# Kernel tuning notes

Hardware: AMD Instinct MI355X
Metric: run time of the kernel (lower is better)

The kernel has to match this reference:

```python
import jax, jax.numpy as jnp
import numpy as np

B, D, N, H = 2, 512, 2048, 8
DK = D // H
EPS = 1e-5


def conv1x1(x, w, b):
    # kernel-size-1 Conv1d == channel-mixing GEMM: (o,i) x (b,i,n) -> (b,o,n)
    return jnp.einsum('oi,bin->bon', w, x) + b[None, :, None]


def setup_inputs() -> dict:
    key = jax.random.key(0)
    ks = jax.random.split(key, 20)
    s = 0.02
    return {
        'init_query': jax.random.normal(ks[0], (B, D, N), jnp.float32),
        'key_t': jax.random.normal(ks[1], (B, D, N), jnp.float32),
        'value': jax.random.normal(ks[2], (B, D, N), jnp.float32),
        'mask': jax.random.randint(ks[3], (B, 1, N, N), 0, 2, jnp.int32),
        'Wq': jax.random.normal(ks[4], (D, D), jnp.float32) * s,
        'bq': jax.random.normal(ks[5], (D,), jnp.float32) * s,
        'Wk': jax.random.normal(ks[6], (D, D), jnp.float32) * s,
        'bk': jax.random.normal(ks[7], (D,), jnp.float32) * s,
        'Wv': jax.random.normal(ks[8], (D, D), jnp.float32) * s,
        'bv': jax.random.normal(ks[9], (D,), jnp.float32) * s,
        'Wm': jax.random.normal(ks[10], (D, D), jnp.float32) * s,
        'bm': jax.random.normal(ks[11], (D,), jnp.float32) * s,
        'W1': jax.random.normal(ks[12], (2 * D, 2 * D), jnp.float32) * s,
        'b1': jax.random.normal(ks[13], (2 * D,), jnp.float32) * s,
        'gamma': jnp.ones((2 * D,), jnp.float32),
        'beta': jnp.zeros((2 * D,), jnp.float32),
        'rmean': jax.random.normal(ks[14], (2 * D,), jnp.float32) * s,
        'rvar': jnp.abs(jax.random.normal(ks[15], (2 * D,), jnp.float32)) * 0.1 + 0.5,
        'W2': jax.random.normal(ks[16], (D, 2 * D), jnp.float32) * s,
        'b2': jnp.zeros((D,), jnp.float32),  # nn.init.constant_(bias, 0.0)
    }


def reference(init_query, key_t, value, mask, Wq, bq, Wk, bk, Wv, bv, Wm, bm,
              W1, b1, gamma, beta, rmean, rvar, W2, b2):
    # projections, split channels into (d_k, n_heads) exactly like torch .view
    q = conv1x1(init_query, Wq, bq).reshape(B, DK, H, N)
    k = conv1x1(key_t, Wk, bk).reshape(B, DK, H, N)
    v = conv1x1(value, Wv, bv).reshape(B, DK, H, N)
    scores = jnp.einsum('bdhn,bdhm->bhnm', q, k) / jnp.sqrt(jnp.float32(DK))
    scores = jnp.where(mask == 0, jnp.float32(-1e9), scores)
    attn = jax.nn.softmax(scores, axis=-1)
    x = jnp.einsum('bhnm,bdhm->bdhn', attn, v).reshape(B, D, N)
    x = conv1x1(x, Wm, bm)
    x = jnp.concatenate([x, init_query], axis=1)  # (B, 2D, N)
    h = conv1x1(x, W1, b1)
    # BatchNorm1d (inference mode with running stats) + ReLU
    h = (h - rmean[None, :, None]) * (gamma / jnp.sqrt(rvar + EPS))[None, :, None] + beta[None, :, None]
    h = jax.nn.relu(h)
    return conv1x1(h, W2, b2)
```

## Files before the change

### kernel.cpp

```cpp
#include <hip/hip_runtime.h>

typedef unsigned short u16;
typedef unsigned int u32;
typedef unsigned long long u64;
typedef long long i64;
typedef __bf16 bf16x8 __attribute__((ext_vector_type(8)));
typedef float f32x4 __attribute__((ext_vector_type(4)));

#define DEV __device__ __forceinline__

constexpr int BB = 2, DD = 512, NN = 2048, HH = 8, DKc = 64, D2 = 1024;

constexpr float QSC = 0.125f * 1.44269504088896340736f;

constexpr i64 OFF_CAT = 0;
constexpr i64 OFF_XKT = 8388608;
constexpr i64 OFF_XVT = 12582912;
constexpr i64 OFF_OP0 = 8388608;
constexpr i64 OFF_QH  = 16777216;
constexpr i64 OFF_KH  = 20971520;
constexpr i64 OFF_VT  = 25165824;
constexpr i64 OFF_OT  = 29360128;
constexpr i64 OFF_HT  = 33554432;
constexpr i64 OFF_OP1 = 33554432;
constexpr i64 OFF_WQP = 41943040;
constexpr i64 OFF_WKP = 42467328;
constexpr i64 OFF_WVP = 42991616;
constexpr i64 OFF_WMP = 43515904;
constexpr i64 OFF_W1B = 44040192;
constexpr i64 OFF_W2B = 46137344;
constexpr i64 OFF_BQP = 47185920;
constexpr i64 OFF_BKP = 47187968;
constexpr i64 OFF_BVP = 47190016;
constexpr i64 OFF_BNA = 47192064;
constexpr i64 OFF_BNC = 47196160;
constexpr i64 OFF_MSK = 47200256;
constexpr i64 OFF_LP  = 48248832;

DEV u16 f2bf(float f) {
  u32 u = __float_as_uint(f);
  u = u + 0x7FFFu + ((u >> 16) & 1u);
  return (u16)(u >> 16);
}

DEV float bf2f(u16 u) { return __uint_as_float(((u32)u) << 16); }

DEV bf16x8 ldfrag(const u16* p) {
  bf16x8 v;
  __builtin_memcpy(&v, __builtin_assume_aligned(p, 16), 16);
  return v;
}

DEV bf16x8 ldfrag8(const u16* p) {
  bf16x8 v;
  __builtin_memcpy(&v, __builtin_assume_aligned(p, 8), 16);
  return v;
}

DEV void gload16(const void* g, void* lds) {
  __builtin_amdgcn_global_load_lds((__attribute__((address_space(1))) void*)g,
                                   (__attribute__((address_space(3))) void*)lds, 16, 0, 0);
}

DEV f32x4 mfma16(bf16x8 a, bf16x8 b, f32x4 c) {
  return __builtin_amdgcn_mfma_f32_16x16x32_bf16(a, b, c, 0, 0, 0);
}

__global__ __launch_bounds__(256) void prep_kernel(
    const float* __restrict__ Wq, const float* __restrict__ Wk, const float* __restrict__ Wv,
    const float* __restrict__ Wm, const float* __restrict__ W1, const float* __restrict__ W2,
    const float* __restrict__ bq, const float* __restrict__ bk, const float* __restrict__ bv,
    const float* __restrict__ b1, const float* __restrict__ gamma_, const float* __restrict__ beta_,
    const float* __restrict__ rmean, const float* __restrict__ rvar, const int* __restrict__ mask,
    u16* __restrict__ wqp, u16* __restrict__ wkp, u16* __restrict__ wvp, u16* __restrict__ wmp,
    u16* __restrict__ w1b, u16* __restrict__ w2b,
    float* __restrict__ bqp, float* __restrict__ bkp, float* __restrict__ bvp,
    float* __restrict__ bna, float* __restrict__ bnc, u32* __restrict__ mw) {
  const int blk = blockIdx.x, t = threadIdx.x;
  if (blk < 768) {
    const int which = blk >> 8, lb = blk & 255;
    const float* W = which == 0 ? Wq : (which == 1 ? Wk : Wv);
    u16* dst = which == 0 ? wqp : (which == 1 ? wkp : wvp);
    for (int e = lb * 256 + t; e < 262144; e += 65536) {
      int op = e >> 9, i = e & 511;
      int dk = op & 63, h = op >> 6;
      dst[e] = f2bf(W[(dk * 8 + h) * 512 + i]);
    }
  } else if (blk < 1024) {
    const int lb = blk - 768;
    for (int e = lb * 256 + t; e < 262144; e += 65536) {
      int o = e >> 9, c = e & 511;
      int dk = c & 63, h = c >> 6;
      wmp[e] = f2bf(Wm[o * 512 + dk * 8 + h]);
    }
  } else if (blk < 1536) {
    const int lb = blk - 1024;
    for (int e = lb * 256 + t; e < 1048576; e += 131072) w1b[e] = f2bf(W1[e]);
  } else if (blk < 1792) {
    const int lb = blk - 1536;
    for (int e = lb * 256 + t; e < 524288; e += 65536) w2b[e] = f2bf(W2[e]);
  } else if (blk == 1792) {
    for (int e = t; e < 512; e += 256) {
      int src = (e & 63) * 8 + (e >> 6);
      bqp[e] = bq[src]; bkp[e] = bk[src]; bvp[e] = bv[src];
    }
    for (int e = t; e < 1024; e += 256) {
      float a = gamma_[e] * rsqrtf(rvar[e] + 1e-5f);
      bna[e] = a;
      bnc[e] = (b1[e] - rmean[e]) * a + beta_[e];
    }
  } else {
    const int tid = (blk - 1793) * 256 + t;
    const i64 base = (i64)tid * 32;
    const int4* mp = (const int4*)(mask + base);
    u32 word = 0;
#pragma unroll
    for (int j = 0; j < 8; ++j) {
      int4 x = mp[j];
      u32 nib = (x.x != 0 ? 1u : 0u) | (x.y != 0 ? 2u : 0u) | (x.z != 0 ? 4u : 0u) |
                (x.w != 0 ? 8u : 0u);
      word |= nib << (j * 4);
    }
    mw[tid] = word;
  }
}

__global__ __launch_bounds__(256) void transpose_cvt(const float* __restrict__ iq,
                                                     const float* __restrict__ kt,
                                                     const float* __restrict__ vv,
                                                     u16* __restrict__ cat, u16* __restrict__ xkt,
                                                     u16* __restrict__ xvt) {
  __shared__ float tile[32][33];
  const int z = blockIdx.z, tensor = z >> 1, b = z & 1;
  const float* src = tensor == 0 ? iq : (tensor == 1 ? kt : vv);
  src += (i64)b * DD * NN;
  u16* dst; i64 ldd; int coff;
  if (tensor == 0)      { dst = cat + (i64)b * NN * D2; ldd = D2; coff = DD; }
  else if (tensor == 1) { dst = xkt + (i64)b * NN * DD; ldd = DD; coff = 0; }
  else                  { dst = xvt + (i64)b * NN * DD; ldd = DD; coff = 0; }
  const int x0 = blockIdx.x * 32, y0 = blockIdx.y * 32;
  const int col = threadIdx.x & 31, rg = threadIdx.x >> 5;
#pragma unroll
  for (int i = 0; i < 4; ++i) {
    int row = rg + i * 8;
    tile[row][col] = src[(i64)(y0 + row) * NN + x0 + col];
  }
  __syncthreads();
#pragma unroll
  for (int i = 0; i < 4; ++i) {
    int rr = rg + i * 8;
    dst[(i64)(x0 + rr) * ldd + coff + y0 + col] = f2bf(tile[col][rr]);
  }
}

struct GArgs {
  const u16* A; i64 lda, sAb;
  const u16* B; i64 ldb, sBb;
  void* C; i64 ldc, sCb;
  const float* p1; const float* p2;
  int K; float sc;
};

template <int MODE>
__global__ __launch_bounds__(256) void gemm_bt(GArgs g) {
  __shared__ __align__(16) u16 As[128 * 64];
  __shared__ __align__(16) u16 Bs[64 * 64];
  const int t = threadIdx.x;
  const int w = t >> 6, l = t & 63, quad = l >> 4, l15 = l & 15;
  const int wm = (w >> 1) * 64, wn = (w & 1) * 32;
  const int bz = blockIdx.z;
  const u16* A = g.A + (i64)bz * g.sAb + (i64)blockIdx.x * 128 * g.lda;
  const u16* Bp = g.B + (i64)bz * g.sBb + (i64)blockIdx.y * 64 * g.ldb;
  f32x4 acc[4][2] = {};
  for (int kk = 0; kk < g.K; kk += 64) {
    __syncthreads();
#pragma unroll
    for (int j = 0; j < 4; ++j) {
      int ch = j * 256 + w * 64 + l, r = ch >> 3, c = ch & 7;
      gload16(A + (i64)r * g.lda + kk + ((c ^ (r & 7)) << 3), &As[(j * 256 + w * 64) * 8]);
    }
#pragma unroll
    for (int j = 0; j < 2; ++j) {
      int ch = j * 256 + w * 64 + l, r = ch >> 3, c = ch & 7;
      gload16(Bp + (i64)r * g.ldb + kk + ((c ^ (r & 7)) << 3), &Bs[(j * 256 + w * 64) * 8]);
    }
    __syncthreads();
#pragma unroll
    for (int kc = 0; kc < 2; ++kc) {
      const int sw = ((kc * 4 + quad) ^ (l15 & 7)) << 3;
      bf16x8 af[4], bfr[2];
#pragma unroll
      for (int i = 0; i < 4; ++i) af[i] = ldfrag(&As[(wm + i * 16 + l15) * 64 + sw]);
#pragma unroll
      for (int j = 0; j < 2; ++j) bfr[j] = ldfrag(&Bs[(wn + j * 16 + l15) * 64 + sw]);
#pragma unroll
      for (int i = 0; i < 4; ++i)
#pragma unroll
        for (int j = 0; j < 2; ++j) acc[i][j] = mfma16(af[i], bfr[j], acc[i][j]);
    }
  }
  const int rowBase = blockIdx.x * 128 + wm + quad * 4;
  const int colBase = blockIdx.y * 64 + wn + l15;
#pragma unroll
  for (int j = 0; j < 2; ++j) {
    const int col = colBase + j * 16;
    float cA = 0.f, cB = 0.f;
    if (MODE == 0 || MODE == 1) cA = g.p1[col];
    if (MODE == 3) { cA = g.p1[col]; cB = g.p2[col]; }
#pragma unroll
    for (int i = 0; i < 4; ++i) {
#pragma unroll
      for (int r = 0; r < 4; ++r) {
        const int row = rowBase + i * 16 + r;
        float v = acc[i][j][r];
        if (MODE == 0) {
          ((u16*)g.C + (i64)bz * g.sCb)[(i64)row * g.ldc + col] = f2bf(v + cA);
        } else if (MODE == 1) {
          ((u16*)g.C + (i64)bz * g.sCb)[(i64)(col >> 6) * (NN * 64) + (i64)row * 64 + (col & 63)] =
              f2bf((v + cA) * g.sc);
        } else if (MODE == 2) {
          ((u16*)g.C + (i64)bz * g.sCb)[(i64)row * g.ldc + col] = f2bf(v + g.p1[row]);
        } else if (MODE == 3) {
          float x = v * cA + cB;
          ((u16*)g.C + (i64)bz * g.sCb)[(i64)row * g.ldc + col] = f2bf(x > 0.f ? x : 0.f);
        } else {
          ((float*)g.C + (i64)bz * g.sCb)[(i64)row * g.ldc + col] = v + g.p1[row];
        }
      }
    }
  }
}

__global__ __launch_bounds__(256) void flash_attn(const u16* __restrict__ Qh,
                                                  const u16* __restrict__ Kh,
                                                  const u16* __restrict__ Vt,
                                                  const u64* __restrict__ MW,
                                                  float* __restrict__ Op0, float* __restrict__ Op1,
                                                  float* __restrict__ Lp) {
  __shared__ __align__(16) u16 Qs[64 * 64];
  __shared__ __align__(16) u16 Ks[64 * 64];
  __shared__ __align__(16) u16 Vs[64 * 64];
  __shared__ __align__(16) u16 Ps[4][16 * 68];
  const int t = threadIdx.x, w = t >> 6, l = t & 63, quad = l >> 4, l15 = l & 15;
  const int nt = blockIdx.x, h = blockIdx.y, zz = blockIdx.z, b = zz >> 1, sp = zz & 1;
  const u16* Qb = Qh + ((i64)(b * HH + h) * NN + nt * 64) * 64;
  const u16* Kb = Kh + (i64)(b * HH + h) * NN * 64;
  const u16* Vb = Vt + (i64)(b * HH + h) * 64 * NN;
#pragma unroll
  for (int j = 0; j < 2; ++j) {
    int ch = j * 256 + w * 64 + l, r = ch >> 3, c = ch & 7;
    gload16(Qb + r * 64 + ((c ^ (r & 7)) << 3), &Qs[(j * 256 + w * 64) * 8]);
  }
  __syncthreads();
  bf16x8 qf[2];
#pragma unroll
  for (int kc = 0; kc < 2; ++kc)
    qf[kc] = ldfrag(&Qs[(w * 16 + l15) * 64 + (((kc * 4 + quad) ^ (l15 & 7)) << 3)]);

  f32x4 oacc[4] = {};
  float lacc[4] = {0.f, 0.f, 0.f, 0.f};
  const int mt0 = sp * 16, mt1 = mt0 + 16;
  for (int mt = mt0; mt < mt1; ++mt) {
    __syncthreads();
#pragma unroll
    for (int j = 0; j < 2; ++j) {
      int ch = j * 256 + w * 64 + l, r = ch >> 3, c = ch & 7;
      gload16(Kb + (i64)mt * 4096 + r * 64 + ((c ^ (r & 7)) << 3), &Ks[(j * 256 + w * 64) * 8]);
      gload16(Vb + (i64)r * NN + mt * 64 + ((c ^ (r & 7)) << 3), &Vs[(j * 256 + w * 64) * 8]);
    }
    __syncthreads();
    f32x4 s[4];
#pragma unroll
    for (int ct = 0; ct < 4; ++ct) {
      const int sw = l15 & 7;
      bf16x8 k0 = ldfrag(&Ks[(ct * 16 + l15) * 64 + ((quad ^ sw) << 3)]);
      bf16x8 k1 = ldfrag(&Ks[(ct * 16 + l15) * 64 + (((4 + quad) ^ sw) << 3)]);
      f32x4 z = {};
      z = mfma16(qf[0], k0, z);
      z = mfma16(qf[1], k1, z);
      s[ct] = z;
    }
    u64 mrow[4];
#pragma unroll
    for (int r = 0; r < 4; ++r) {
      int n = nt * 64 + w * 16 + quad * 4 + r;
      mrow[r] = MW[(i64)(b * NN + n) * 32 + mt];
    }
#pragma unroll
    for (int ct = 0; ct < 4; ++ct)
#pragma unroll
      for (int r = 0; r < 4; ++r) {
        float p = ((mrow[r] >> (ct * 16 + l15)) & 1ull) ? exp2f(s[ct][r]) : 0.f;
        lacc[r] += p;
        Ps[w][(quad * 4 + r) * 68 + ct * 16 + l15] = f2bf(p);
      }
    asm volatile("" ::: "memory");
    bf16x8 pf0 = ldfrag8(&Ps[w][l15 * 68 + quad * 8]);
    bf16x8 pf1 = ldfrag8(&Ps[w][l15 * 68 + 32 + quad * 8]);
#pragma unroll
    for (int dt = 0; dt < 4; ++dt) {
      const int sw = l15 & 7;
      bf16x8 v0 = ldfrag(&Vs[(dt * 16 + l15) * 64 + ((quad ^ sw) << 3)]);
      bf16x8 v1 = ldfrag(&Vs[(dt * 16 + l15) * 64 + (((4 + quad) ^ sw) << 3)]);
      oacc[dt] = mfma16(pf0, v0, oacc[dt]);
      oacc[dt] = mfma16(pf1, v1, oacc[dt]);
    }
  }
#pragma unroll
  for (int off = 1; off < 16; off <<= 1)
#pragma unroll
    for (int r = 0; r < 4; ++r) lacc[r] += __shfl_xor(lacc[r], off);
  float* Op = sp ? Op1 : Op0;
#pragma unroll
  for (int dt = 0; dt < 4; ++dt)
#pragma unroll
    for (int r = 0; r < 4; ++r) {
      int n = nt * 64 + w * 16 + quad * 4 + r;
      Op[((i64)(b * HH + h) * NN + n) * 64 + dt * 16 + l15] = oacc[dt][r];
    }
  if (l15 == 0) {
#pragma unroll
    for (int r = 0; r < 4; ++r) {
      int n = nt * 64 + w * 16 + quad * 4 + r;
      Lp[(i64)sp * BB * HH * NN + (i64)(b * HH + h) * NN + n] = lacc[r];
    }
  }
}

__global__ __launch_bounds__(256) void combine(const float* __restrict__ Op0,
                                               const float* __restrict__ Op1,
                                               const float* __restrict__ Lp,
                                               u16* __restrict__ Ot) {
  int idx = blockIdx.x * 256 + threadIdx.x;
  int b = idx >> 20, rem = idx & ((1 << 20) - 1);
  int n = rem >> 9, ch = rem & 511, h = ch >> 6, dk = ch & 63;
  i64 o = ((i64)(b * HH + h) * NN + n) * 64 + dk;
  float l0 = Lp[(i64)(b * HH + h) * NN + n];
  float l1 = Lp[(i64)BB * HH * NN + (i64)(b * HH + h) * NN + n];
  Ot[(i64)(b * NN + n) * DD + ch] = f2bf((Op0[o] + Op1[o]) / (l0 + l1));
}

extern "C" void kernel_launch(void* const* d_in, const int* in_sizes, int n_in,
                              void* d_out, int out_size, void* d_ws, size_t ws_size,
                              hipStream_t stream) {
  (void)in_sizes; (void)n_in; (void)out_size; (void)ws_size;
  const float* iq    = (const float*)d_in[0];
  const float* kt    = (const float*)d_in[1];
  const float* vv    = (const float*)d_in[2];
  const int*   mask  = (const int*)d_in[3];
  const float* Wq    = (const float*)d_in[4];
  const float* bq    = (const float*)d_in[5];
  const float* Wk    = (const float*)d_in[6];
  const float* bk    = (const float*)d_in[7];
  const float* Wv    = (const float*)d_in[8];
  const float* bv    = (const float*)d_in[9];
  const float* Wm    = (const float*)d_in[10];
  const float* bm    = (const float*)d_in[11];
  const float* W1    = (const float*)d_in[12];
  const float* b1    = (const float*)d_in[13];
  const float* gamma_= (const float*)d_in[14];
  const float* beta_ = (const float*)d_in[15];
  const float* rmean = (const float*)d_in[16];
  const float* rvar  = (const float*)d_in[17];
  const float* W2    = (const float*)d_in[18];
  const float* b2    = (const float*)d_in[19];

  char* ws = (char*)d_ws;
  u16* cat = (u16*)(ws + OFF_CAT);
  u16* xkt = (u16*)(ws + OFF_XKT);
  u16* xvt = (u16*)(ws + OFF_XVT);
  u16* qh  = (u16*)(ws + OFF_QH);
  u16* kh  = (u16*)(ws + OFF_KH);
  u16* vt  = (u16*)(ws + OFF_VT);
  u16* ot  = (u16*)(ws + OFF_OT);
  u16* ht  = (u16*)(ws + OFF_HT);
  u16* wqp = (u16*)(ws + OFF_WQP);
  u16* wkp = (u16*)(ws + OFF_WKP);
  u16* wvp = (u16*)(ws + OFF_WVP);
  u16* wmp = (u16*)(ws + OFF_WMP);
  u16* w1b = (u16*)(ws + OFF_W1B);
  u16* w2b = (u16*)(ws + OFF_W2B);
  float* bqp = (float*)(ws + OFF_BQP);
  float* bkp = (float*)(ws + OFF_BKP);
  float* bvp = (float*)(ws + OFF_BVP);
  float* bna = (float*)(ws + OFF_BNA);
  float* bnc = (float*)(ws + OFF_BNC);
  u32* mw = (u32*)(ws + OFF_MSK);
  float* op0 = (float*)(ws + OFF_OP0);
  float* op1 = (float*)(ws + OFF_OP1);
  float* lp  = (float*)(ws + OFF_LP);

  prep_kernel<<<2817, 256, 0, stream>>>(Wq, Wk, Wv, Wm, W1, W2, bq, bk, bv, b1, gamma_, beta_,
                                        rmean, rvar, mask, wqp, wkp, wvp, wmp, w1b, w2b,
                                        bqp, bkp, bvp, bna, bnc, mw);
  transpose_cvt<<<dim3(64, 16, 6), 256, 0, stream>>>(iq, kt, vv, cat, xkt, xvt);

  GArgs qa{cat + DD, D2, (i64)NN * D2, wqp, DD, 0, qh, 0, (i64)HH * NN * DKc, bqp, nullptr, DD, QSC};
  gemm_bt<1><<<dim3(16, 8, 2), 256, 0, stream>>>(qa);
  GArgs ka{xkt, DD, (i64)NN * DD, wkp, DD, 0, kh, 0, (i64)HH * NN * DKc, bkp, nullptr, DD, 1.f};
  gemm_bt<1><<<dim3(16, 8, 2), 256, 0, stream>>>(ka);
  GArgs va{wvp, DD, 0, xvt, DD, (i64)NN * DD, vt, NN, (i64)HH * DKc * NN, bvp, nullptr, DD, 1.f};
  gemm_bt<2><<<dim3(4, 32, 2), 256, 0, stream>>>(va);

  flash_attn<<<dim3(32, 8, 4), 256, 0, stream>>>(qh, kh, vt, (const u64*)mw, op0, op1, lp);
  combine<<<8192, 256, 0, stream>>>(op0, op1, lp, ot);

  GArgs ma{ot, DD, (i64)NN * DD, wmp, DD, 0, cat, D2, (i64)NN * D2, bm, nullptr, DD, 1.f};
  gemm_bt<0><<<dim3(16, 8, 2), 256, 0, stream>>>(ma);
  GArgs wa{cat, D2, (i64)NN * D2, w1b, D2, 0, ht, D2, (i64)NN * D2, bna, bnc, D2, 1.f};
  gemm_bt<3><<<dim3(16, 16, 2), 256, 0, stream>>>(wa);
  GArgs w2a{w2b, D2, 0, ht, D2, (i64)NN * D2, d_out, NN, (i64)DD * NN, b2, nullptr, D2, 1.f};
  gemm_bt<4><<<dim3(4, 32, 2), 256, 0, stream>>>(w2a);
}
```

Measured before the change: 262.0 us.

## Fuse QKV GEMMs, drop attention split-K combine, compute row sums via MFMA

The three Q/K/V projection GEMMs become one launch indexed by blockIdx.z. Flash attention no longer splits the key range in two, so it drops the fp32 partial outputs and the separate combine kernel and writes normalized bf16 output directly. Inside attention, masking is applied with packed bitwise ANDs on bf16 pairs. Row sums of P are now taken with an MFMA against a ones vector instead of a shuffle reduction. The V output uses a permuted column layout to allow vector stores of P, and the Wm and W2 GEMMs use smaller tiles for more blocks. In exchange, attention has half as many blocks, each with a loop twice as long.

```diff
diff --git a/kernel.cpp b/kernel.cpp
--- a/kernel.cpp
+++ b/kernel.cpp
@@ -5,6 +5,8 @@
 typedef unsigned long long u64;
 typedef long long i64;
 typedef __bf16 bf16x8 __attribute__((ext_vector_type(8)));
+typedef u16 u16x8 __attribute__((ext_vector_type(8)));
+typedef u32 u32x2 __attribute__((ext_vector_type(2)));
 typedef float f32x4 __attribute__((ext_vector_type(4)));
 
 #define DEV __device__ __forceinline__
@@ -16,13 +18,11 @@
 constexpr i64 OFF_CAT = 0;
 constexpr i64 OFF_XKT = 8388608;
 constexpr i64 OFF_XVT = 12582912;
-constexpr i64 OFF_OP0 = 8388608;
 constexpr i64 OFF_QH  = 16777216;
 constexpr i64 OFF_KH  = 20971520;
 constexpr i64 OFF_VT  = 25165824;
 constexpr i64 OFF_OT  = 29360128;
 constexpr i64 OFF_HT  = 33554432;
-constexpr i64 OFF_OP1 = 33554432;
 constexpr i64 OFF_WQP = 41943040;
 constexpr i64 OFF_WKP = 42467328;
 constexpr i64 OFF_WVP = 42991616;
@@ -35,7 +35,6 @@
 constexpr i64 OFF_BNA = 47192064;
 constexpr i64 OFF_BNC = 47196160;
 constexpr i64 OFF_MSK = 47200256;
-constexpr i64 OFF_LP  = 48248832;
 
 DEV u16 f2bf(float f) {
   u32 u = __float_as_uint(f);
@@ -43,7 +42,17 @@
   return (u16)(u >> 16);
 }
 
-DEV float bf2f(u16 u) { return __uint_as_float(((u32)u) << 16); }
+DEV u32 packbf(float lo, float hi) {
+  return __builtin_amdgcn_perm(__float_as_uint(hi), __float_as_uint(lo), 0x07060302u);
+}
+
+DEV float fexp2(float x) {
+#if __has_builtin(__builtin_amdgcn_exp2f)
+  return __builtin_amdgcn_exp2f(x);
+#else
+  return exp2f(x);
+#endif
+}
 
 DEV bf16x8 ldfrag(const u16* p) {
   bf16x8 v;
@@ -54,6 +63,13 @@
 DEV bf16x8 ldfrag8(const u16* p) {
   bf16x8 v;
   __builtin_memcpy(&v, __builtin_assume_aligned(p, 8), 16);
+  return v;
+}
+
+DEV bf16x8 ones8() {
+  u16x8 u = {0x3F80, 0x3F80, 0x3F80, 0x3F80, 0x3F80, 0x3F80, 0x3F80, 0x3F80};
+  bf16x8 v;
+  __builtin_memcpy(&v, &u, 16);
   return v;
 }
 
@@ -153,73 +169,148 @@
   }
 }
 
+template <int AM, int AN>
+DEV void gemm_core(const u16* __restrict__ A, i64 lda, const u16* __restrict__ Bp, i64 ldb,
+                   int K, u16* As, u16* Bs, f32x4 (&acc)[AM][AN]) {
+  constexpr int BM = AM * 32, BN = AN * 32;
+  const int t = threadIdx.x, w = t >> 6, l = t & 63, quad = l >> 4, l15 = l & 15;
+  const int wm = (w >> 1) * AM * 16, wn = (w & 1) * AN * 16;
+  for (int kk = 0; kk < K; kk += 64) {
+    __syncthreads();
+#pragma unroll
+    for (int j = 0; j < BM / 32; ++j) {
+      int ch = j * 256 + w * 64 + l, r = ch >> 3, c = ch & 7;
+      gload16(A + (i64)r * lda + kk + ((c ^ (r & 7)) << 3), As + (j * 256 + w * 64) * 8);
+    }
+#pragma unroll
+    for (int j = 0; j < BN / 32; ++j) {
+      int ch = j * 256 + w * 64 + l, r = ch >> 3, c = ch & 7;
+      gload16(Bp + (i64)r * ldb + kk + ((c ^ (r & 7)) << 3), Bs + (j * 256 + w * 64) * 8);
+    }
+    __syncthreads();
+#pragma unroll
+    for (int kc = 0; kc < 2; ++kc) {
+      const int sw = ((kc * 4 + quad) ^ (l15 & 7)) << 3;
+      bf16x8 af[AM], bfr[AN];
+#pragma unroll
+      for (int i = 0; i < AM; ++i) af[i] = ldfrag(&As[(wm + i * 16 + l15) * 64 + sw]);
+#pragma unroll
+      for (int j = 0; j < AN; ++j) bfr[j] = ldfrag(&Bs[(wn + j * 16 + l15) * 64 + sw]);
+#pragma unroll
+      for (int i = 0; i < AM; ++i)
+#pragma unroll
+        for (int j = 0; j < AN; ++j) acc[i][j] = mfma16(af[i], bfr[j], acc[i][j]);
+    }
+  }
+}
+
+__global__ __launch_bounds__(256) void qkv_gemm(const u16* __restrict__ cat,
+                                                const u16* __restrict__ xkt,
+                                                const u16* __restrict__ xvt,
+                                                const u16* __restrict__ wqp,
+                                                const u16* __restrict__ wkp,
+                                                const u16* __restrict__ wvp,
+                                                const float* __restrict__ bqp,
+                                                const float* __restrict__ bkp,
+                                                const float* __restrict__ bvp,
+                                                u16* __restrict__ qh, u16* __restrict__ kh,
+                                                u16* __restrict__ vt) {
+  __shared__ __align__(16) u16 As[128 * 64];
+  __shared__ __align__(16) u16 Bs[64 * 64];
+  const int z = blockIdx.z, op = z >> 1, b = z & 1;
+  const int t = threadIdx.x, w = t >> 6, l = t & 63, quad = l >> 4, l15 = l & 15;
+  const int wm = (w >> 1) * 64, wn = (w & 1) * 32;
+  int mx, ny;
+  const u16 *A, *Bp;
+  i64 lda, ldb;
+  if (op < 2) {
+    mx = blockIdx.x; ny = blockIdx.y;
+    A = (op == 0 ? cat + DD : xkt);
+    lda = (op == 0 ? D2 : DD);
+    A += (i64)b * NN * lda + (i64)mx * 128 * lda;
+    Bp = (op == 0 ? wqp : wkp) + (i64)ny * 64 * DD;
+    ldb = DD;
+  } else {
+    int f = blockIdx.x * 8 + blockIdx.y;
+    mx = f >> 5; ny = f & 31;
+    A = wvp + (i64)mx * 128 * DD; lda = DD;
+    Bp = xvt + (i64)b * NN * DD + (i64)ny * 64 * DD; ldb = DD;
+  }
+  f32x4 acc[4][2] = {};
+  gemm_core<4, 2>(A, lda, Bp, ldb, DD, As, Bs, acc);
+
+  const int rowBase = mx * 128 + wm + quad * 4;
+  const int colBase = ny * 64 + wn + l15;
+  if (op < 2) {
+    const float* bias = (op == 0 ? bqp : bkp);
+    const float sc = (op == 0 ? QSC : 1.f);
+    u16* dst = (op == 0 ? qh : kh) + (i64)b * HH * NN * DKc;
+#pragma unroll
+    for (int j = 0; j < 2; ++j) {
+      const int col = colBase + j * 16;
+      const float cA = bias[col];
+#pragma unroll
+      for (int i = 0; i < 4; ++i)
+#pragma unroll
+        for (int r = 0; r < 4; ++r) {
+          const int row = rowBase + i * 16 + r;
+          dst[(i64)(col >> 6) * (NN * 64) + (i64)row * 64 + (col & 63)] =
+              f2bf((acc[i][j][r] + cA) * sc);
+        }
+    }
+  } else {
+    u16* dst = vt + (i64)b * HH * DKc * NN;
+#pragma unroll
+    for (int j = 0; j < 2; ++j) {
+      const int col = colBase + j * 16;
+      const int colp = (col & ~63) | (((col & 15) << 2) | ((col >> 4) & 3));
+#pragma unroll
+      for (int i = 0; i < 4; ++i)
+#pragma unroll
+        for (int r = 0; r < 4; ++r) {
+          const int row = rowBase + i * 16 + r;
+          dst[(i64)row * NN + colp] = f2bf(acc[i][j][r] + bvp[row]);
+        }
+    }
+  }
+}
+
 struct GArgs {
   const u16* A; i64 lda, sAb;
   const u16* B; i64 ldb, sBb;
   void* C; i64 ldc, sCb;
   const float* p1; const float* p2;
-  int K; float sc;
+  int K;
 };
 
-template <int MODE>
+template <int MODE, int AM, int AN>
 __global__ __launch_bounds__(256) void gemm_bt(GArgs g) {
-  __shared__ __align__(16) u16 As[128 * 64];
-  __shared__ __align__(16) u16 Bs[64 * 64];
-  const int t = threadIdx.x;
-  const int w = t >> 6, l = t & 63, quad = l >> 4, l15 = l & 15;
-  const int wm = (w >> 1) * 64, wn = (w & 1) * 32;
+  __shared__ __align__(16) u16 As[AM * 32 * 64];
+  __shared__ __align__(16) u16 Bs[AN * 32 * 64];
+  const int t = threadIdx.x, w = t >> 6, l = t & 63, quad = l >> 4, l15 = l & 15;
+  const int wm = (w >> 1) * AM * 16, wn = (w & 1) * AN * 16;
   const int bz = blockIdx.z;
-  const u16* A = g.A + (i64)bz * g.sAb + (i64)blockIdx.x * 128 * g.lda;
-  const u16* Bp = g.B + (i64)bz * g.sBb + (i64)blockIdx.y * 64 * g.ldb;
-  f32x4 acc[4][2] = {};
-  for (int kk = 0; kk < g.K; kk += 64) {
-    __syncthreads();
-#pragma unroll
-    for (int j = 0; j < 4; ++j) {
-      int ch = j * 256 + w * 64 + l, r = ch >> 3, c = ch & 7;
-      gload16(A + (i64)r * g.lda + kk + ((c ^ (r & 7)) << 3), &As[(j * 256 + w * 64) * 8]);
-    }
-#pragma unroll
-    for (int j = 0; j < 2; ++j) {
-      int ch = j * 256 + w * 64 + l, r = ch >> 3, c = ch & 7;
-      gload16(Bp + (i64)r * g.ldb + kk + ((c ^ (r & 7)) << 3), &Bs[(j * 256 + w * 64) * 8]);
-    }
-    __syncthreads();
-#pragma unroll
-    for (int kc = 0; kc < 2; ++kc) {
-      const int sw = ((kc * 4 + quad) ^ (l15 & 7)) << 3;
-      bf16x8 af[4], bfr[2];
-#pragma unroll
-      for (int i = 0; i < 4; ++i) af[i] = ldfrag(&As[(wm + i * 16 + l15) * 64 + sw]);
-#pragma unroll
-      for (int j = 0; j < 2; ++j) bfr[j] = ldfrag(&Bs[(wn + j * 16 + l15) * 64 + sw]);
-#pragma unroll
-      for (int i = 0; i < 4; ++i)
-#pragma unroll
-        for (int j = 0; j < 2; ++j) acc[i][j] = mfma16(af[i], bfr[j], acc[i][j]);
-    }
-  }
-  const int rowBase = blockIdx.x * 128 + wm + quad * 4;
-  const int colBase = blockIdx.y * 64 + wn + l15;
-#pragma unroll
-  for (int j = 0; j < 2; ++j) {
+  const u16* A = g.A + (i64)bz * g.sAb + (i64)blockIdx.x * (AM * 32) * g.lda;
+  const u16* Bp = g.B + (i64)bz * g.sBb + (i64)blockIdx.y * (AN * 32) * g.ldb;
+  f32x4 acc[AM][AN] = {};
+  gemm_core<AM, AN>(A, g.lda, Bp, g.ldb, g.K, As, Bs, acc);
+
+  const int rowBase = blockIdx.x * (AM * 32) + wm + quad * 4;
+  const int colBase = blockIdx.y * (AN * 32) + wn + l15;
+#pragma unroll
+  for (int j = 0; j < AN; ++j) {
     const int col = colBase + j * 16;
     float cA = 0.f, cB = 0.f;
-    if (MODE == 0 || MODE == 1) cA = g.p1[col];
+    if (MODE == 0) cA = g.p1[col];
     if (MODE == 3) { cA = g.p1[col]; cB = g.p2[col]; }
 #pragma unroll
-    for (int i = 0; i < 4; ++i) {
+    for (int i = 0; i < AM; ++i) {
 #pragma unroll
       for (int r = 0; r < 4; ++r) {
         const int row = rowBase + i * 16 + r;
         float v = acc[i][j][r];
         if (MODE == 0) {
           ((u16*)g.C + (i64)bz * g.sCb)[(i64)row * g.ldc + col] = f2bf(v + cA);
-        } else if (MODE == 1) {
-          ((u16*)g.C + (i64)bz * g.sCb)[(i64)(col >> 6) * (NN * 64) + (i64)row * 64 + (col & 63)] =
-              f2bf((v + cA) * g.sc);
-        } else if (MODE == 2) {
-          ((u16*)g.C + (i64)bz * g.sCb)[(i64)row * g.ldc + col] = f2bf(v + g.p1[row]);
         } else if (MODE == 3) {
           float x = v * cA + cB;
           ((u16*)g.C + (i64)bz * g.sCb)[(i64)row * g.ldc + col] = f2bf(x > 0.f ? x : 0.f);
@@ -235,17 +326,17 @@
                                                   const u16* __restrict__ Kh,
                                                   const u16* __restrict__ Vt,
                                                   const u64* __restrict__ MW,
-                                                  float* __restrict__ Op0, float* __restrict__ Op1,
-                                                  float* __restrict__ Lp) {
+                                                  u16* __restrict__ Ot) {
   __shared__ __align__(16) u16 Qs[64 * 64];
   __shared__ __align__(16) u16 Ks[64 * 64];
   __shared__ __align__(16) u16 Vs[64 * 64];
   __shared__ __align__(16) u16 Ps[4][16 * 68];
   const int t = threadIdx.x, w = t >> 6, l = t & 63, quad = l >> 4, l15 = l & 15;
-  const int nt = blockIdx.x, h = blockIdx.y, zz = blockIdx.z, b = zz >> 1, sp = zz & 1;
+  const int nt = blockIdx.x, h = blockIdx.y, b = blockIdx.z;
   const u16* Qb = Qh + ((i64)(b * HH + h) * NN + nt * 64) * 64;
   const u16* Kb = Kh + (i64)(b * HH + h) * NN * 64;
   const u16* Vb = Vt + (i64)(b * HH + h) * 64 * NN;
+  const bf16x8 ONE = ones8();
 #pragma unroll
   for (int j = 0; j < 2; ++j) {
     int ch = j * 256 + w * 64 + l, r = ch >> 3, c = ch & 7;
@@ -258,9 +349,8 @@
     qf[kc] = ldfrag(&Qs[(w * 16 + l15) * 64 + (((kc * 4 + quad) ^ (l15 & 7)) << 3)]);
 
   f32x4 oacc[4] = {};
-  float lacc[4] = {0.f, 0.f, 0.f, 0.f};
-  const int mt0 = sp * 16, mt1 = mt0 + 16;
-  for (int mt = mt0; mt < mt1; ++mt) {
+  f32x4 lacc = {};
+  for (int mt = 0; mt < NN / 64; ++mt) {
     __syncthreads();
 #pragma unroll
     for (int j = 0; j < 2; ++j) {
@@ -280,23 +370,22 @@
       z = mfma16(qf[1], k1, z);
       s[ct] = z;
     }
-    u64 mrow[4];
 #pragma unroll
     for (int r = 0; r < 4; ++r) {
       int n = nt * 64 + w * 16 + quad * 4 + r;
-      mrow[r] = MW[(i64)(b * NN + n) * 32 + mt];
-    }
-#pragma unroll
-    for (int ct = 0; ct < 4; ++ct)
-#pragma unroll
-      for (int r = 0; r < 4; ++r) {
-        float p = ((mrow[r] >> (ct * 16 + l15)) & 1ull) ? exp2f(s[ct][r]) : 0.f;
-        lacc[r] += p;
-        Ps[w][(quad * 4 + r) * 68 + ct * 16 + l15] = f2bf(p);
-      }
+      u64 sh = MW[(i64)(b * NN + n) * 32 + mt] >> l15;
+      u32 m01 = ((u32)sh & 0x00010001u) * 0xFFFFu;
+      u32 m23 = ((u32)(sh >> 32) & 0x00010001u) * 0xFFFFu;
+      u32 w0 = packbf(fexp2(s[0][r]), fexp2(s[1][r])) & m01;
+      u32 w1 = packbf(fexp2(s[2][r]), fexp2(s[3][r])) & m23;
+      u32x2 pair = {w0, w1};
+      __builtin_memcpy(__builtin_assume_aligned(&Ps[w][(quad * 4 + r) * 68 + l15 * 4], 8), &pair, 8);
+    }
     asm volatile("" ::: "memory");
     bf16x8 pf0 = ldfrag8(&Ps[w][l15 * 68 + quad * 8]);
     bf16x8 pf1 = ldfrag8(&Ps[w][l15 * 68 + 32 + quad * 8]);
+    lacc = mfma16(pf0, ONE, lacc);
+    lacc = mfma16(pf1, ONE, lacc);
 #pragma unroll
     for (int dt = 0; dt < 4; ++dt) {
       const int sw = l15 & 7;
@@ -306,38 +395,16 @@
       oacc[dt] = mfma16(pf1, v1, oacc[dt]);
     }
   }
-#pragma unroll
-  for (int off = 1; off < 16; off <<= 1)
-#pragma unroll
-    for (int r = 0; r < 4; ++r) lacc[r] += __shfl_xor(lacc[r], off);
-  float* Op = sp ? Op1 : Op0;
+  float inv[4];
+#pragma unroll
+  for (int r = 0; r < 4; ++r) inv[r] = __builtin_amdgcn_rcpf(lacc[r]);
 #pragma unroll
   for (int dt = 0; dt < 4; ++dt)
 #pragma unroll
     for (int r = 0; r < 4; ++r) {
       int n = nt * 64 + w * 16 + quad * 4 + r;
-      Op[((i64)(b * HH + h) * NN + n) * 64 + dt * 16 + l15] = oacc[dt][r];
-    }
-  if (l15 == 0) {
-#pragma unroll
-    for (int r = 0; r < 4; ++r) {
-      int n = nt * 64 + w * 16 + quad * 4 + r;
-      Lp[(i64)sp * BB * HH * NN + (i64)(b * HH + h) * NN + n] = lacc[r];
-    }
-  }
-}
-
-__global__ __launch_bounds__(256) void combine(const float* __restrict__ Op0,
-                                               const float* __restrict__ Op1,
-                                               const float* __restrict__ Lp,
-                                               u16* __restrict__ Ot) {
-  int idx = blockIdx.x * 256 + threadIdx.x;
-  int b = idx >> 20, rem = idx & ((1 << 20) - 1);
-  int n = rem >> 9, ch = rem & 511, h = ch >> 6, dk = ch & 63;
-  i64 o = ((i64)(b * HH + h) * NN + n) * 64 + dk;
-  float l0 = Lp[(i64)(b * HH + h) * NN + n];
-  float l1 = Lp[(i64)BB * HH * NN + (i64)(b * HH + h) * NN + n];
-  Ot[(i64)(b * NN + n) * DD + ch] = f2bf((Op0[o] + Op1[o]) / (l0 + l1));
+      Ot[((i64)b * NN + n) * DD + h * DKc + dt * 16 + l15] = f2bf(oacc[dt][r] * inv[r]);
+    }
 }
 
 extern "C" void kernel_launch(void* const* d_in, const int* in_sizes, int n_in,
@@ -386,29 +453,21 @@
   float* bna = (float*)(ws + OFF_BNA);
   float* bnc = (float*)(ws + OFF_BNC);
   u32* mw = (u32*)(ws + OFF_MSK);
-  float* op0 = (float*)(ws + OFF_OP0);
-  float* op1 = (float*)(ws + OFF_OP1);
-  float* lp  = (float*)(ws + OFF_LP);
 
   prep_kernel<<<2817, 256, 0, stream>>>(Wq, Wk, Wv, Wm, W1, W2, bq, bk, bv, b1, gamma_, beta_,
                                         rmean, rvar, mask, wqp, wkp, wvp, wmp, w1b, w2b,
                                         bqp, bkp, bvp, bna, bnc, mw);
   transpose_cvt<<<dim3(64, 16, 6), 256, 0, stream>>>(iq, kt, vv, cat, xkt, xvt);
 
-  GArgs qa{cat + DD, D2, (i64)NN * D2, wqp, DD, 0, qh, 0, (i64)HH * NN * DKc, bqp, nullptr, DD, QSC};
-  gemm_bt<1><<<dim3(16, 8, 2), 256, 0, stream>>>(qa);
-  GArgs ka{xkt, DD, (i64)NN * DD, wkp, DD, 0, kh, 0, (i64)HH * NN * DKc, bkp, nullptr, DD, 1.f};
-  gemm_bt<1><<<dim3(16, 8, 2), 256, 0, stream>>>(ka);
-  GArgs va{wvp, DD, 0, xvt, DD, (i64)NN * DD, vt, NN, (i64)HH * DKc * NN, bvp, nullptr, DD, 1.f};
-  gemm_bt<2><<<dim3(4, 32, 2), 256, 0, stream>>>(va);
-
-  flash_attn<<<dim3(32, 8, 4), 256, 0, stream>>>(qh, kh, vt, (const u64*)mw, op0, op1, lp);
-  combine<<<8192, 256, 0, stream>>>(op0, op1, lp, ot);
-
-  GArgs ma{ot, DD, (i64)NN * DD, wmp, DD, 0, cat, D2, (i64)NN * D2, bm, nullptr, DD, 1.f};
-  gemm_bt<0><<<dim3(16, 8, 2), 256, 0, stream>>>(ma);
-  GArgs wa{cat, D2, (i64)NN * D2, w1b, D2, 0, ht, D2, (i64)NN * D2, bna, bnc, D2, 1.f};
-  gemm_bt<3><<<dim3(16, 16, 2), 256, 0, stream>>>(wa);
-  GArgs w2a{w2b, D2, 0, ht, D2, (i64)NN * D2, d_out, NN, (i64)DD * NN, b2, nullptr, D2, 1.f};
-  gemm_bt<4><<<dim3(4, 32, 2), 256, 0, stream>>>(w2a);
-}
+  qkv_gemm<<<dim3(16, 8, 6), 256, 0, stream>>>(cat, xkt, xvt, wqp, wkp, wvp, bqp, bkp, bvp,
+                                               qh, kh, vt);
+
+  flash_attn<<<dim3(32, 8, 2), 256, 0, stream>>>(qh, kh, vt, (const u64*)mw, ot);
+
+  GArgs ma{ot, DD, (i64)NN * DD, wmp, DD, 0, cat, D2, (i64)NN * D2, bm, nullptr, DD};
+  gemm_bt<0, 2, 2><<<dim3(32, 8, 2), 256, 0, stream>>>(ma);
+  GArgs wa{cat, D2, (i64)NN * D2, w1b, D2, 0, ht, D2, (i64)NN * D2, bna, bnc, D2};
+  gemm_bt<3, 4, 2><<<dim3(16, 16, 2), 256, 0, stream>>>(wa);
+  GArgs w2a{w2b, D2, 0, ht, D2, (i64)NN * D2, d_out, NN, (i64)DD * NN, b2, nullptr, D2};
+  gemm_bt<4, 2, 2><<<dim3(8, 32, 2), 256, 0, stream>>>(w2a);
+}
```

New measurement: 233.5 us. 10.9% less time.
